# Kernel optimization log

Measured on AMD Instinct MI355X. Metric: run time of the kernel, lower is better.

## Reference

```python
import jax, jax.numpy as jnp
import numpy as np
import math

B = 256        # batch of series
V = 1024       # vocabulary size (Vocabulary not given; modeled as V random words)
SIZE = 1024    # self.size
CELL = 8       # self.cell_size == word length
SEQ = SIZE // CELL   # 128 segments
DMODEL = 768
NHAAR = 8      # int(log2(128)) + 1
THRESH = 0.95


def _pos_emb():
    position = np.arange(SEQ, dtype=np.float32)[:, None]
    div = np.exp(np.arange(0, DMODEL, 2, dtype=np.float32) * (-math.log(10000.0) / DMODEL))
    pe = np.zeros((SEQ, DMODEL), np.float32)
    pe[:, 0::2] = np.sin(position * div)
    pe[:, 1::2] = np.cos(position * div)
    return jnp.asarray(pe)


def setup_inputs() -> dict:
    key = jax.random.key(0)
    k1, k2, k3, k4 = jax.random.split(key, 4)
    return {
        "X": jax.random.normal(k1, (B, SIZE), jnp.float32),
        "vocab": jax.random.normal(k2, (V, CELL), jnp.float32),
        "word_emb": jax.random.normal(k3, (V, DMODEL), jnp.float32),
        "haar_emb": jax.random.normal(k4, (NHAAR, DMODEL), jnp.float32),
        "pos_emb": _pos_emb(),
    }


def _select(corr):
    """Replicates get_sequence's sequential update over vocabulary order.
    Stored best is the SIGNED correlation c (faithful to the original code),
    compared against |c_new|; accept when |c_new| > threshold and best < |c_new|.
    corr: [B, V, S] -> idx [B, S] (int32, -1 = no word selected)."""
    cs = jnp.transpose(corr, (1, 0, 2))  # [V, B, S]

    def step(carry, xs):
        best, idx = carry
        c, i = xs
        a = jnp.abs(c)
        take = (a > THRESH) & (best < a)
        return (jnp.where(take, c, best), jnp.where(take, i, idx)), None

    init = (jnp.full((corr.shape[0], corr.shape[2]), -jnp.inf, corr.dtype),
            jnp.full((corr.shape[0], corr.shape[2]), -1, jnp.int32))
    (_, idx), _ = jax.lax.scan(step, init, (cs, jnp.arange(V, dtype=jnp.int32)))
    return idx


def _haar_details(x):
    """pywt 'haar' detail coeffs: ds[k] = cD_{k+1}, cD = (x_even - x_odd)/sqrt(2)."""
    inv = jnp.float32(1.0 / math.sqrt(2.0))
    a = x
    ds = []
    for _ in range(10):  # log2(1024) levels
        ds.append((a[:, ::2] - a[:, 1::2]) * inv)
        a = (a[:, ::2] + a[:, 1::2]) * inv
    return ds


def reference(X, vocab, word_emb, haar_emb, pos_emb):
    # --- per-segment cross-correlation against every vocabulary word ---
    seg = X.reshape(B, SEQ, CELL)
    seg_c = seg - seg.mean(-1, keepdims=True)
    seg_std = jnp.sqrt((seg_c * seg_c).mean(-1))          # population std, [B,S]
    w_c = vocab - vocab.mean(-1, keepdims=True)
    w_std = jnp.sqrt((w_c * w_c).mean(-1))                # [V]
    cov = jnp.einsum('bsc,vc->bvs', seg_c, w_c) / CELL    # [B,V,S]
    denom = w_std[None, :, None] * seg_std[:, None, :]
    corr = jnp.where(denom == 0, 0.0, cov / jnp.where(denom == 0, 1.0, denom))

    idx = _select(corr)                                   # [B,S]
    mask = (idx >= 0)

    # --- word embedding lookup (zeros where no word passed threshold) ---
    we = word_emb[jnp.clip(idx, 0, V - 1)] * mask[..., None].astype(word_emb.dtype)

    # --- Haar wavelet coefficients, levels cD_10 .. cD_3 (lengths 1..128) ---
    ds = _haar_details(X)
    pos = jnp.arange(SEQ)
    cols = []
    for l in range(NHAAR):                                # haar_coeffs[l] = cD_{10-l}
        gi = (pos * (2 ** l)) // SEQ                      # i // (SEQ / 2**l)
        cols.append(ds[9 - l][:, gi])                     # [B,S]
    hc = jnp.stack(cols, axis=-1) * mask[..., None].astype(X.dtype)  # [B,S,8]
    haar = jnp.einsum('bsh,hd->bsd', hc, haar_emb)        # [B,S,768]

    return we + pos_emb[None] + haar                      # [B,128,768]
```

## Files before the change

kernel.cpp:

```cpp
#include <hip/hip_runtime.h>
#include <math.h>

#define THRESH_ 0.95f

typedef __attribute__((ext_vector_type(8))) short short8v;
typedef __attribute__((ext_vector_type(16))) float f32x16;

__device__ __forceinline__ unsigned short f2bf_rne(float x) {
    unsigned u = __float_as_uint(x);
    u += 0x7fffu + ((u >> 16) & 1u);
    return (unsigned short)(u >> 16);
}

__global__ __launch_bounds__(1024) void k12_fused(const float* __restrict__ X,
                                                  const float* __restrict__ vocab,
                                                  const float* __restrict__ word_emb,
                                                  const float* __restrict__ haar_emb,
                                                  const float* __restrict__ pos_emb,
                                                  float* __restrict__ out) {
    __shared__ float4  wcl4[2048];
    __shared__ short8v wcb_lds[1024];
    __shared__ float   wsl[1024];
    __shared__ float   xrow[1024];
    __shared__ float   segf[1024];
    __shared__ short8v segb[128];
    __shared__ float   sstd_l[128];
    __shared__ float   thr_l[128];
    __shared__ float   stb[512];
    __shared__ int     sti[512];
    __shared__ float   stm[512];
    __shared__ float   tree[254];
    __shared__ float   hc_lds[1024];
    __shared__ int     idx_lds[128];

    int t = threadIdx.x;
    int b = blockIdx.x;

    xrow[t] = X[b * 1024 + t];
    {
        const float4* v4 = (const float4*)vocab + t * 2;
        float4 a = v4[0], bb = v4[1];
        float w[8] = {a.x, a.y, a.z, a.w, bb.x, bb.y, bb.z, bb.w};
        float s = 0.f;
#pragma unroll
        for (int c = 0; c < 8; c++) s += w[c];
        float mean = s * 0.125f;
        float ss = 0.f;
        float wcv[8];
#pragma unroll
        for (int c = 0; c < 8; c++) { wcv[c] = w[c] - mean; ss += wcv[c] * wcv[c]; }
        float sd = sqrtf(ss * 0.125f);
        float4 o0 = {wcv[0], wcv[1], wcv[2], wcv[3]};
        float4 o1 = {wcv[4], wcv[5], wcv[6], wcv[7]};
        wcl4[t * 2] = o0;
        wcl4[t * 2 + 1] = o1;
        wsl[t] = sd;
        union { uint4 q; unsigned short u[8]; } pk;
#pragma unroll
        for (int c = 0; c < 8; c++) pk.u[c] = f2bf_rne(wcv[c]);
        ((uint4*)wcb_lds)[t] = pk.q;
    }
    if (t < 512) { stb[t] = -INFINITY; sti[t] = -1; stm[t] = 0.f; }
    __syncthreads();

    if (t < 128) {
        float seg[8];
#pragma unroll
        for (int c = 0; c < 8; c++) seg[c] = xrow[t * 8 + c];
        float sum = 0.f;
#pragma unroll
        for (int c = 0; c < 8; c++) sum += seg[c];
        float mean = sum * 0.125f;
        float segc[8];
        float ss = 0.f;
#pragma unroll
        for (int c = 0; c < 8; c++) { segc[c] = seg[c] - mean; ss += segc[c] * segc[c]; }
        float sstd = sqrtf(ss * 0.125f);
        union { short8v v; unsigned short u[8]; } pk;
#pragma unroll
        for (int c = 0; c < 8; c++) { segf[t * 8 + c] = segc[c]; pk.u[c] = f2bf_rne(segc[c]); }
        segb[t] = pk.v;
        sstd_l[t] = sstd;
        thr_l[t] = 7.52f * sstd;
        tree[t] = sum;
    }
    __syncthreads();

    int w = t >> 6, lane = t & 63;
    {
        int sb = w & 3;
        int g = w >> 2;
        int half = lane >> 5;

        short8v af = {0, 0, 0, 0, 0, 0, 0, 0};
        if (lane < 32) af = segb[sb * 32 + lane];

        float thr_r[16];
#pragma unroll
        for (int i = 0; i < 16; i++) {
            int row = (i & 3) + 8 * (i >> 2) + 4 * half;
            thr_r[i] = thr_l[sb * 32 + row];
        }

        const double MID = 0x1.E66667p-1;
        for (int j = 0; j < 8; j++) {
            int wb = g * 8 + j;
            short8v bf = {0, 0, 0, 0, 0, 0, 0, 0};
            if (lane < 32) bf = wcb_lds[wb * 32 + lane];
            float wsd_c = wsl[wb * 32 + (lane & 31)];

            f32x16 accz = {0.f, 0.f, 0.f, 0.f, 0.f, 0.f, 0.f, 0.f,
                           0.f, 0.f, 0.f, 0.f, 0.f, 0.f, 0.f, 0.f};
            f32x16 acc = __builtin_amdgcn_mfma_f32_32x32x16_bf16(af, bf, accz, 0, 0, 0);

            bool anyp = false;
#pragma unroll
            for (int i = 0; i < 16; i++) anyp |= (fabsf(acc[i]) > thr_r[i] * wsd_c);

            if (__builtin_expect(anyp, 0)) {
#pragma unroll
                for (int i = 0; i < 16; i++) {
                    unsigned long long mi = __ballot(fabsf(acc[i]) > thr_r[i] * wsd_c);
                    while (mi) {
                        int src = __builtin_ctzll(mi);
                        mi &= mi - 1;
                        if (lane == src) {
                            int col = src & 31;
                            int seg_r = sb * 32 + (i & 3) + 8 * (i >> 2) + 4 * (src >> 5);
                            int v = wb * 32 + col;
                            float sst = sstd_l[seg_r];
                            float wsd = wsl[v];
                            const float* sc = &segf[seg_r * 8];
                            float4 wa = wcl4[v * 2];
                            float4 wbv = wcl4[v * 2 + 1];
                            float dot = sc[0] * wa.x + sc[1] * wa.y + sc[2] * wa.z + sc[3] * wa.w
                                      + sc[4] * wbv.x + sc[5] * wbv.y + sc[6] * wbv.z + sc[7] * wbv.w;
                            float cov = dot * 0.125f;
                            float denom = wsd * sst;
                            if ((double)fabsf(cov) >= MID * (double)denom) {
                                float c = (denom == 0.f) ? 0.f : cov / denom;
                                float a = fabsf(c);
                                int sidx = g * 128 + seg_r;
                                stm[sidx] = fmaxf(stm[sidx], a);
                                if (a > THRESH_ && stb[sidx] < a) { stb[sidx] = c; sti[sidx] = v; }
                            }
                        }
                    }
                }
            }
        }
    }
    __syncthreads();

    if (t < 64) tree[128 + t] = tree[2 * t] + tree[2 * t + 1];
    __syncthreads();
    if (t < 32) tree[192 + t] = tree[128 + 2 * t] + tree[128 + 2 * t + 1];
    __syncthreads();
    if (t < 16) tree[224 + t] = tree[192 + 2 * t] + tree[192 + 2 * t + 1];
    __syncthreads();
    if (t < 8) tree[240 + t] = tree[224 + 2 * t] + tree[224 + 2 * t + 1];
    __syncthreads();
    if (t < 4) tree[248 + t] = tree[240 + 2 * t] + tree[240 + 2 * t + 1];
    __syncthreads();
    if (t < 2) tree[252 + t] = tree[248 + 2 * t] + tree[248 + 2 * t + 1];
    __syncthreads();

    if (t < 128) {
        float Bb = stb[t];
        int I = sti[t];
#pragma unroll
        for (int p = 1; p < 4; p++) {
            float yb = stb[p * 128 + t];
            int yi = sti[p * 128 + t];
            float ym = stm[p * 128 + t];
            bool take = (yi != -1) && (!(Bb > THRESH_) || (ym > Bb));
            if (take) { Bb = yb; I = yi; }
        }
        float mask = (I >= 0) ? 1.f : 0.f;

        const int base[7] = {252, 248, 240, 224, 192, 128, 0};
        const float scl[7] = {0.03125f, 0.04419417382415922f, 0.0625f,
                              0.08838834764831843f, 0.125f,
                              0.17677669529663687f, 0.25f};
        float hcv[8];
#pragma unroll
        for (int l = 0; l < 7; l++) {
            int j = (t << l) >> 7;
            hcv[l] = scl[l] * (tree[base[l] + 2 * j] - tree[base[l] + 2 * j + 1]);
        }
        float s4a = xrow[t * 8 + 0] + xrow[t * 8 + 1] + xrow[t * 8 + 2] + xrow[t * 8 + 3];
        float s4b = xrow[t * 8 + 4] + xrow[t * 8 + 5] + xrow[t * 8 + 6] + xrow[t * 8 + 7];
        hcv[7] = 0.3535533905932738f * (s4a - s4b);

#pragma unroll
        for (int l = 0; l < 8; l++) hc_lds[t * 8 + l] = hcv[l] * mask;
        idx_lds[t] = I;
    }
    __syncthreads();

    if (w < 12) {
        int third = w % 3;
        int grp = w / 3;
        int c = third * 64 + lane;

        float4 he[8];
        const float4* hg = (const float4*)haar_emb;
#pragma unroll
        for (int l = 0; l < 8; l++) he[l] = hg[l * 192 + c];

        const float4* pos4 = (const float4*)pos_emb;
        const float4* we4 = (const float4*)word_emb;
        float4* out4 = (float4*)out + (size_t)b * 128 * 192;

        for (int k = 0; k < 32; k += 2) {
            int row0 = grp * 32 + k;
            int row1 = row0 + 1;
            int iv0 = idx_lds[row0];
            int iv1 = idx_lds[row1];
            int ivc0 = iv0 < 0 ? 0 : iv0;
            int ivc1 = iv1 < 0 ? 0 : iv1;
            float msk0 = iv0 < 0 ? 0.f : 1.f;
            float msk1 = iv1 < 0 ? 0.f : 1.f;
            float4 p0 = pos4[row0 * 192 + c];
            float4 w0 = we4[(size_t)ivc0 * 192 + c];
            float4 h0a = *(const float4*)&hc_lds[row0 * 8];
            float4 h0b = *(const float4*)&hc_lds[row0 * 8 + 4];
            float4 p1 = pos4[row1 * 192 + c];
            float4 w1 = we4[(size_t)ivc1 * 192 + c];
            float4 h1a = *(const float4*)&hc_lds[row1 * 8];
            float4 h1b = *(const float4*)&hc_lds[row1 * 8 + 4];

            float4 acc0;
            acc0.x = fmaf(w0.x, msk0, p0.x);
            acc0.y = fmaf(w0.y, msk0, p0.y);
            acc0.z = fmaf(w0.z, msk0, p0.z);
            acc0.w = fmaf(w0.w, msk0, p0.w);
            float h0[8] = {h0a.x, h0a.y, h0a.z, h0a.w, h0b.x, h0b.y, h0b.z, h0b.w};
#pragma unroll
            for (int l = 0; l < 8; l++) {
                acc0.x += h0[l] * he[l].x;
                acc0.y += h0[l] * he[l].y;
                acc0.z += h0[l] * he[l].z;
                acc0.w += h0[l] * he[l].w;
            }
            out4[row0 * 192 + c] = acc0;

            float4 acc1;
            acc1.x = fmaf(w1.x, msk1, p1.x);
            acc1.y = fmaf(w1.y, msk1, p1.y);
            acc1.z = fmaf(w1.z, msk1, p1.z);
            acc1.w = fmaf(w1.w, msk1, p1.w);
            float h1[8] = {h1a.x, h1a.y, h1a.z, h1a.w, h1b.x, h1b.y, h1b.z, h1b.w};
#pragma unroll
            for (int l = 0; l < 8; l++) {
                acc1.x += h1[l] * he[l].x;
                acc1.y += h1[l] * he[l].y;
                acc1.z += h1[l] * he[l].z;
                acc1.w += h1[l] * he[l].w;
            }
            out4[row1 * 192 + c] = acc1;
        }
    }
}

extern "C" void kernel_launch(void* const* d_in, const int* in_sizes, int n_in,
                              void* d_out, int out_size, void* d_ws, size_t ws_size,
                              hipStream_t stream) {
    const float* X        = (const float*)d_in[0];
    const float* vocab    = (const float*)d_in[1];
    const float* word_emb = (const float*)d_in[2];
    const float* haar_emb = (const float*)d_in[3];
    const float* pos_emb  = (const float*)d_in[4];
    float* out = (float*)d_out;

    hipLaunchKernelGGL(k12_fused, dim3(256), dim3(1024), 0, stream,
                       X, vocab, word_emb, haar_emb, pos_emb, out);
}
```

Before: 36.21 us.

## Halve block size to 512 threads and redistribute work across all waves

Launches 512-thread blocks instead of 1024. Each thread now does two vocab rows of preprocessing, each wave covers two word groups in the MFMA correlation scan, and the output stage uses all 8 waves at 16 rows each instead of 12 waves. The aim is better occupancy and register headroom through launch bounds (512,4), and using every wave during the memory-bound output write. The trade-off is more serial work per wave and haar_emb reloaded per row instead of held in registers.

Measured after the change: 40.95 us. 1.13x slower.

```diff
diff --git a/kernel.cpp b/kernel.cpp
--- a/kernel.cpp
+++ b/kernel.cpp
@@ -12,12 +12,12 @@
     return (unsigned short)(u >> 16);
 }
 
-__global__ __launch_bounds__(1024) void k12_fused(const float* __restrict__ X,
-                                                  const float* __restrict__ vocab,
-                                                  const float* __restrict__ word_emb,
-                                                  const float* __restrict__ haar_emb,
-                                                  const float* __restrict__ pos_emb,
-                                                  float* __restrict__ out) {
+__global__ __launch_bounds__(512, 4) void k12_fused(const float* __restrict__ X,
+                                                    const float* __restrict__ vocab,
+                                                    const float* __restrict__ word_emb,
+                                                    const float* __restrict__ haar_emb,
+                                                    const float* __restrict__ pos_emb,
+                                                    float* __restrict__ out) {
     __shared__ float4  wcl4[2048];
     __shared__ short8v wcb_lds[1024];
     __shared__ float   wsl[1024];
@@ -37,8 +37,11 @@
     int b = blockIdx.x;
 
     xrow[t] = X[b * 1024 + t];
-    {
-        const float4* v4 = (const float4*)vocab + t * 2;
+    xrow[t + 512] = X[b * 1024 + t + 512];
+#pragma unroll
+    for (int rep = 0; rep < 2; rep++) {
+        int v = t + rep * 512;
+        const float4* v4 = (const float4*)vocab + v * 2;
         float4 a = v4[0], bb = v4[1];
         float w[8] = {a.x, a.y, a.z, a.w, bb.x, bb.y, bb.z, bb.w};
         float s = 0.f;
@@ -52,15 +55,15 @@
         float sd = sqrtf(ss * 0.125f);
         float4 o0 = {wcv[0], wcv[1], wcv[2], wcv[3]};
         float4 o1 = {wcv[4], wcv[5], wcv[6], wcv[7]};
-        wcl4[t * 2] = o0;
-        wcl4[t * 2 + 1] = o1;
-        wsl[t] = sd;
+        wcl4[v * 2] = o0;
+        wcl4[v * 2 + 1] = o1;
+        wsl[v] = sd;
         union { uint4 q; unsigned short u[8]; } pk;
 #pragma unroll
         for (int c = 0; c < 8; c++) pk.u[c] = f2bf_rne(wcv[c]);
-        ((uint4*)wcb_lds)[t] = pk.q;
-    }
-    if (t < 512) { stb[t] = -INFINITY; sti[t] = -1; stm[t] = 0.f; }
+        ((uint4*)wcb_lds)[v] = pk.q;
+    }
+    { stb[t] = -INFINITY; sti[t] = -1; stm[t] = 0.f; }
     __syncthreads();
 
     if (t < 128) {
@@ -89,7 +92,7 @@
     int w = t >> 6, lane = t & 63;
     {
         int sb = w & 3;
-        int g = w >> 2;
+        int gp = w >> 2;
         int half = lane >> 5;
 
         short8v af = {0, 0, 0, 0, 0, 0, 0, 0};
@@ -103,46 +106,49 @@
         }
 
         const double MID = 0x1.E66667p-1;
-        for (int j = 0; j < 8; j++) {
-            int wb = g * 8 + j;
-            short8v bf = {0, 0, 0, 0, 0, 0, 0, 0};
-            if (lane < 32) bf = wcb_lds[wb * 32 + lane];
-            float wsd_c = wsl[wb * 32 + (lane & 31)];
-
-            f32x16 accz = {0.f, 0.f, 0.f, 0.f, 0.f, 0.f, 0.f, 0.f,
-                           0.f, 0.f, 0.f, 0.f, 0.f, 0.f, 0.f, 0.f};
-            f32x16 acc = __builtin_amdgcn_mfma_f32_32x32x16_bf16(af, bf, accz, 0, 0, 0);
-
-            bool anyp = false;
-#pragma unroll
-            for (int i = 0; i < 16; i++) anyp |= (fabsf(acc[i]) > thr_r[i] * wsd_c);
-
-            if (__builtin_expect(anyp, 0)) {
-#pragma unroll
-                for (int i = 0; i < 16; i++) {
-                    unsigned long long mi = __ballot(fabsf(acc[i]) > thr_r[i] * wsd_c);
-                    while (mi) {
-                        int src = __builtin_ctzll(mi);
-                        mi &= mi - 1;
-                        if (lane == src) {
-                            int col = src & 31;
-                            int seg_r = sb * 32 + (i & 3) + 8 * (i >> 2) + 4 * (src >> 5);
-                            int v = wb * 32 + col;
-                            float sst = sstd_l[seg_r];
-                            float wsd = wsl[v];
-                            const float* sc = &segf[seg_r * 8];
-                            float4 wa = wcl4[v * 2];
-                            float4 wbv = wcl4[v * 2 + 1];
-                            float dot = sc[0] * wa.x + sc[1] * wa.y + sc[2] * wa.z + sc[3] * wa.w
-                                      + sc[4] * wbv.x + sc[5] * wbv.y + sc[6] * wbv.z + sc[7] * wbv.w;
-                            float cov = dot * 0.125f;
-                            float denom = wsd * sst;
-                            if ((double)fabsf(cov) >= MID * (double)denom) {
-                                float c = (denom == 0.f) ? 0.f : cov / denom;
-                                float a = fabsf(c);
-                                int sidx = g * 128 + seg_r;
-                                stm[sidx] = fmaxf(stm[sidx], a);
-                                if (a > THRESH_ && stb[sidx] < a) { stb[sidx] = c; sti[sidx] = v; }
+        for (int gg = 0; gg < 2; gg++) {
+            int g = gp * 2 + gg;
+            for (int j = 0; j < 8; j++) {
+                int wb = g * 8 + j;
+                short8v bf = {0, 0, 0, 0, 0, 0, 0, 0};
+                if (lane < 32) bf = wcb_lds[wb * 32 + lane];
+                float wsd_c = wsl[wb * 32 + (lane & 31)];
+
+                f32x16 accz = {0.f, 0.f, 0.f, 0.f, 0.f, 0.f, 0.f, 0.f,
+                               0.f, 0.f, 0.f, 0.f, 0.f, 0.f, 0.f, 0.f};
+                f32x16 acc = __builtin_amdgcn_mfma_f32_32x32x16_bf16(af, bf, accz, 0, 0, 0);
+
+                bool anyp = false;
+#pragma unroll
+                for (int i = 0; i < 16; i++) anyp |= (fabsf(acc[i]) > thr_r[i] * wsd_c);
+
+                if (__builtin_expect(anyp, 0)) {
+#pragma unroll
+                    for (int i = 0; i < 16; i++) {
+                        unsigned long long mi = __ballot(fabsf(acc[i]) > thr_r[i] * wsd_c);
+                        while (mi) {
+                            int src = __builtin_ctzll(mi);
+                            mi &= mi - 1;
+                            if (lane == src) {
+                                int col = src & 31;
+                                int seg_r = sb * 32 + (i & 3) + 8 * (i >> 2) + 4 * (src >> 5);
+                                int v = wb * 32 + col;
+                                float sst = sstd_l[seg_r];
+                                float wsd = wsl[v];
+                                const float* sc = &segf[seg_r * 8];
+                                float4 wa = wcl4[v * 2];
+                                float4 wbv = wcl4[v * 2 + 1];
+                                float dot = sc[0] * wa.x + sc[1] * wa.y + sc[2] * wa.z + sc[3] * wa.w
+                                          + sc[4] * wbv.x + sc[5] * wbv.y + sc[6] * wbv.z + sc[7] * wbv.w;
+                                float cov = dot * 0.125f;
+                                float denom = wsd * sst;
+                                if ((double)fabsf(cov) >= MID * (double)denom) {
+                                    float c = (denom == 0.f) ? 0.f : cov / denom;
+                                    float a = fabsf(c);
+                                    int sidx = g * 128 + seg_r;
+                                    stm[sidx] = fmaxf(stm[sidx], a);
+                                    if (a > THRESH_ && stb[sidx] < a) { stb[sidx] = c; sti[sidx] = v; }
+                                }
                             }
                         }
                     }
@@ -198,67 +204,48 @@
     }
     __syncthreads();
 
-    if (w < 12) {
-        int third = w % 3;
-        int grp = w / 3;
-        int c = third * 64 + lane;
-
-        float4 he[8];
-        const float4* hg = (const float4*)haar_emb;
-#pragma unroll
-        for (int l = 0; l < 8; l++) he[l] = hg[l * 192 + c];
-
+    {
         const float4* pos4 = (const float4*)pos_emb;
         const float4* we4 = (const float4*)word_emb;
+        const float4* hg = (const float4*)haar_emb;
         float4* out4 = (float4*)out + (size_t)b * 128 * 192;
 
-        for (int k = 0; k < 32; k += 2) {
-            int row0 = grp * 32 + k;
-            int row1 = row0 + 1;
-            int iv0 = idx_lds[row0];
-            int iv1 = idx_lds[row1];
-            int ivc0 = iv0 < 0 ? 0 : iv0;
-            int ivc1 = iv1 < 0 ? 0 : iv1;
-            float msk0 = iv0 < 0 ? 0.f : 1.f;
-            float msk1 = iv1 < 0 ? 0.f : 1.f;
-            float4 p0 = pos4[row0 * 192 + c];
-            float4 w0 = we4[(size_t)ivc0 * 192 + c];
-            float4 h0a = *(const float4*)&hc_lds[row0 * 8];
-            float4 h0b = *(const float4*)&hc_lds[row0 * 8 + 4];
-            float4 p1 = pos4[row1 * 192 + c];
-            float4 w1 = we4[(size_t)ivc1 * 192 + c];
-            float4 h1a = *(const float4*)&hc_lds[row1 * 8];
-            float4 h1b = *(const float4*)&hc_lds[row1 * 8 + 4];
-
-            float4 acc0;
-            acc0.x = fmaf(w0.x, msk0, p0.x);
-            acc0.y = fmaf(w0.y, msk0, p0.y);
-            acc0.z = fmaf(w0.z, msk0, p0.z);
-            acc0.w = fmaf(w0.w, msk0, p0.w);
-            float h0[8] = {h0a.x, h0a.y, h0a.z, h0a.w, h0b.x, h0b.y, h0b.z, h0b.w};
-#pragma unroll
-            for (int l = 0; l < 8; l++) {
-                acc0.x += h0[l] * he[l].x;
-                acc0.y += h0[l] * he[l].y;
-                acc0.z += h0[l] * he[l].z;
-                acc0.w += h0[l] * he[l].w;
+        for (int k = 0; k < 16; k++) {
+            int row = w * 16 + k;
+            int iv = idx_lds[row];
+            int ivc = iv < 0 ? 0 : iv;
+            float msk = iv < 0 ? 0.f : 1.f;
+            float4 ha = *(const float4*)&hc_lds[row * 8];
+            float4 hb = *(const float4*)&hc_lds[row * 8 + 4];
+            float h[8] = {ha.x, ha.y, ha.z, ha.w, hb.x, hb.y, hb.z, hb.w};
+
+            float4 p0 = pos4[row * 192 + lane];
+            float4 p1 = pos4[row * 192 + 64 + lane];
+            float4 p2 = pos4[row * 192 + 128 + lane];
+            float4 w0 = we4[(size_t)ivc * 192 + lane];
+            float4 w1 = we4[(size_t)ivc * 192 + 64 + lane];
+            float4 w2 = we4[(size_t)ivc * 192 + 128 + lane];
+
+#pragma unroll
+            for (int third = 0; third < 3; third++) {
+                int c = third * 64 + lane;
+                float4 p = third == 0 ? p0 : (third == 1 ? p1 : p2);
+                float4 wv = third == 0 ? w0 : (third == 1 ? w1 : w2);
+                float4 acc;
+                acc.x = fmaf(wv.x, msk, p.x);
+                acc.y = fmaf(wv.y, msk, p.y);
+                acc.z = fmaf(wv.z, msk, p.z);
+                acc.w = fmaf(wv.w, msk, p.w);
+#pragma unroll
+                for (int l = 0; l < 8; l++) {
+                    float4 he = hg[l * 192 + c];
+                    acc.x += h[l] * he.x;
+                    acc.y += h[l] * he.y;
+                    acc.z += h[l] * he.z;
+                    acc.w += h[l] * he.w;
+                }
+                out4[row * 192 + c] = acc;
             }
-            out4[row0 * 192 + c] = acc0;
-
-            float4 acc1;
-            acc1.x = fmaf(w1.x, msk1, p1.x);
-            acc1.y = fmaf(w1.y, msk1, p1.y);
-            acc1.z = fmaf(w1.z, msk1, p1.z);
-            acc1.w = fmaf(w1.w, msk1, p1.w);
-            float h1[8] = {h1a.x, h1a.y, h1a.z, h1a.w, h1b.x, h1b.y, h1b.z, h1b.w};
-#pragma unroll
-            for (int l = 0; l < 8; l++) {
-                acc1.x += h1[l] * he[l].x;
-                acc1.y += h1[l] * he[l].y;
-                acc1.z += h1[l] * he[l].z;
-                acc1.w += h1[l] * he[l].w;
-            }
-            out4[row1 * 192 + c] = acc1;
         }
     }
 }
@@ -273,6 +260,6 @@
     const float* pos_emb  = (const float*)d_in[4];
     float* out = (float*)d_out;
 
-    hipLaunchKernelGGL(k12_fused, dim3(256), dim3(1024), 0, stream,
+    hipLaunchKernelGGL(k12_fused, dim3(256), dim3(512), 0, stream,
                        X, vocab, word_emb, haar_emb, pos_emb, out);
 }
```
